# Performance work log

Measured on AMD Instinct MI355X. Metric: run time of the kernel, lower is better.

Reference implementation:

```python
import jax, jax.numpy as jnp
import numpy as np

N = 2060          # drug-graph nodes (m_drug_d_num)
F_OUT = 901       # out_feats, forced by Linear(901*2, ...)
M = 901 + (N - 1183)  # 1778 fused node rows
E = N * 64
N_TRAIN, N_TEST = 100000, 30000
EPS = 1e-5


def setup_inputs() -> dict:
    key = jax.random.key(0)
    ks = jax.random.split(key, 30)
    f32 = jnp.float32
    inp = {
        'x_feat': jax.random.normal(ks[0], (N, N), f32),
        'mirna_feat': jax.random.normal(ks[1], (M, F_OUT), f32),
        'Wg': jax.random.normal(ks[2], (N, F_OUT), f32) * 0.02,
        'att_src': jax.random.normal(ks[3], (F_OUT,), f32) * 0.05,
        'att_dst': jax.random.normal(ks[4], (F_OUT,), f32) * 0.05,
        'gat_b': jnp.zeros((F_OUT,), f32),
        'lw1': jax.random.normal(ks[5], (1, 2), f32) * 0.5,
        'lb1': jnp.zeros((1,), f32),
        'lw2': jax.random.normal(ks[6], (2, 1), f32) * 0.5,
        'lb2': jnp.zeros((2,), f32),
        'gw1': jax.random.normal(ks[7], (1, 2), f32) * 0.5,
        'gb1': jnp.zeros((1,), f32),
        'gw2': jax.random.normal(ks[8], (2, 1), f32) * 0.5,
        'gb2': jnp.zeros((2,), f32),
        'W1': jax.random.normal(ks[9], (2 * F_OUT, 1024), f32) * 0.02,
        'b1': jnp.zeros((1024,), f32),
        'W2': jax.random.normal(ks[10], (1024, 512), f32) * 0.03,
        'b2': jnp.zeros((512,), f32),
        'W3': jax.random.normal(ks[11], (512, 64), f32) * 0.04,
        'b3': jnp.zeros((64,), f32),
        'W4': jax.random.normal(ks[12], (64, 1), f32) * 0.1,
        'b4': jnp.zeros((1,), f32),
        'edge_index': jax.random.randint(ks[13], (2, E), 0, N, jnp.int32),
        'train_sample': jax.random.randint(ks[14], (N_TRAIN, 2), 0, M, jnp.int32),
        'test_sample': jax.random.randint(ks[15], (N_TEST, 2), 0, M, jnp.int32),
    }
    return inp


def _bn(x, axes):
    # BatchNorm in train mode (fresh module: gamma=1, beta=0, biased batch var)
    mu = x.mean(axes, keepdims=True)
    var = x.var(axes, keepdims=True)
    return (x - mu) * jax.lax.rsqrt(var + EPS)


def _gat(x, Wg, att_src, att_dst, gat_b, edge_index):
    # single-head PyG-style GATConv with self loops, negative_slope=0.2
    h = x @ Wg                                         # [N, F]
    loop = jnp.arange(N, dtype=edge_index.dtype)
    src = jnp.concatenate([edge_index[0], loop])
    dst = jnp.concatenate([edge_index[1], loop])
    a_s = h @ att_src                                  # [N]
    a_d = h @ att_dst
    e = jax.nn.leaky_relu(a_s[src] + a_d[dst], 0.2)    # per-edge logits
    emax = jax.ops.segment_max(e, dst, num_segments=N)
    ex = jnp.exp(e - emax[dst])
    denom = jax.ops.segment_sum(ex, dst, num_segments=N)
    alpha = ex / denom[dst]
    out = jax.ops.segment_sum(alpha[:, None] * h[src], dst, num_segments=N) + gat_b
    return jax.nn.relu(out)                            # F.relu in MGL (MGC relu is idempotent)


def _forward(x_feat, mirna_feat, Wg, att_src, att_dst, gat_b,
             lw1, lb1, lw2, lb2, gw1, gb1, gw2, gb2,
             W1, b1, W2, b2, W3, b3, W4, b4,
             edge_index, train_sample, test_sample):
    g = _gat(x_feat, Wg, att_src, att_dst, gat_b, edge_index)      # [N, 901]
    drug_view = jnp.concatenate([g[:901], g[1183:]], axis=0)       # [M, 901]
    x = jnp.stack([drug_view, mirna_feat], axis=1)                 # [M, 2, 901]  (B=M, C=2, H=1 dropped, W=901)

    # MS_CAM (channels=2, r=2), BN in train mode
    xl = jnp.einsum('mcw,oc->mow', x, lw1) + lb1[None, :, None]    # [M, 1, 901]
    xl = jax.nn.relu(_bn(xl, (0, 2)))
    xl = jnp.einsum('mcw,oc->mow', xl, lw2) + lb2[None, :, None]   # [M, 2, 901]
    xl = _bn(xl, (0, 2))

    gp = x.mean(axis=2)                                            # [M, 2] global avg pool
    xg = gp @ gw1.T + gb1                                          # [M, 1]
    xg = jax.nn.relu(_bn(xg, (0,)))
    xg = xg @ gw2.T + gb2                                          # [M, 2]
    xg = _bn(xg, (0,))

    wei = jax.nn.sigmoid(xl + xg[:, :, None])
    x = x * wei                                                    # [M, 2, 901]
    fused = (x[:, 0, :] + x[:, 1, :]) * 0.5                        # [M, 901]

    def score(pairs):
        emb = jnp.concatenate([fused[pairs[:, 0]], fused[pairs[:, 1]]], axis=1)  # [B, 1802]
        h = emb @ W1 + b1
        h = h @ W2 + b2
        h = h @ W3 + b3
        return jax.nn.sigmoid(h @ W4 + b4)

    return score(train_sample), score(test_sample)


def reference(x_feat, mirna_feat, Wg, att_src, att_dst, gat_b,
              lw1, lb1, lw2, lb2, gw1, gb1, gw2, gb2,
              W1, b1, W2, b2, W3, b3, W4, b4,
              edge_index, train_sample, test_sample):
    return _forward(x_feat, mirna_feat, Wg, att_src, att_dst, gat_b,
                    lw1, lb1, lw2, lb2, gw1, gb1, gw2, gb2,
                    W1, b1, W2, b2, W3, b3, W4, b4,
                    edge_index, train_sample, test_sample)
```

## Files before the change

kernel.cpp:

```cpp
#include <hip/hip_runtime.h>

typedef unsigned short u16;
typedef unsigned int   u32;

#define NN   2060
#define FF   901
#define HP   904
#define MM   1778
#define EE   131840
#define ETOT 133900
#define NTR  100000
#define NOUT 130000
#define MP   2112
#define KP   2080
#define NP   960
#define EPSV 1e-5f
#define NTOT 1601978.0

typedef __attribute__((ext_vector_type(4))) float f32x4;
typedef __attribute__((ext_vector_type(8))) short bf16x8;

#define GLL16(g,l) __builtin_amdgcn_global_load_lds( \
    (const __attribute__((address_space(1))) u32*)(g), \
    (__attribute__((address_space(3))) u32*)(l), 16, 0, 0)

__device__ __forceinline__ float bf2f(u16 u){ return __uint_as_float(((u32)u)<<16); }
__device__ __forceinline__ u16 f2bf(float f){
  u32 b = __float_as_uint(f);
  return (u16)((b + 0x7fffu + ((b>>16)&1u)) >> 16);
}
__device__ __forceinline__ float ldf(const void* p, size_t i, int bf){
  return bf ? bf2f(((const u16*)p)[i]) : ((const float*)p)[i];
}
__device__ __forceinline__ u16 ldb(const void* p, size_t i, int bf){
  return bf ? ((const u16*)p)[i] : f2bf(((const float*)p)[i]);
}
__device__ __forceinline__ float waveSum(float v){
  #pragma unroll
  for (int o = 32; o; o >>= 1) v += __shfl_down(v, o);
  return v;
}
__device__ __forceinline__ int waveSumI(int v){
  #pragma unroll
  for (int o = 32; o; o >>= 1) v += __shfl_down(v, o);
  return v;
}
__device__ __forceinline__ int flagWave(const u32* __restrict__ x){
  int l = threadIdx.x & 63;
  u32 w0 = x[l], w1 = x[l + 64];
  int big = (((w0 >> 7)  & 0xFFu) >= 0xC0u) + (((w0 >> 23) & 0xFFu) >= 0xC0u)
          + (((w1 >> 7)  & 0xFFu) >= 0xC0u) + (((w1 >> 23) & 0xFFu) >= 0xC0u);
  big = waveSumI(big);
  return (__shfl(big, 0) >= 8) ? 0 : 1;
}
__device__ __forceinline__ void edgeSD(const int* __restrict__ ei, int e, int& src, int& dst){
  if (e < EE){ src = ei[e]; dst = ei[EE + e]; } else { src = dst = e - EE; }
}

__global__ __launch_bounds__(256) void pad_k(const void* __restrict__ X, const void* __restrict__ Wg,
                                             const void* __restrict__ W3, const void* __restrict__ W4,
                                             const void* __restrict__ b3, const void* __restrict__ b4,
                                             const int* __restrict__ ei,
                                             u16* __restrict__ Ap, u16* __restrict__ BT,
                                             float* __restrict__ u3, float* __restrict__ cp,
                                             int* __restrict__ cnts, int* bfp){
  __shared__ u16 tt[32][33];
  int bf = flagWave((const u32*)X);
  int blk = blockIdx.x, tid = threadIdx.x;
  if (blk == 0 && tid == 0) *bfp = bf;
  if (blk < MP){
    int row = blk;
    for (int c0 = tid * 8; c0 < KP; c0 += 2048){
      u16 v[8] = {0,0,0,0,0,0,0,0};
      if (row < NN){
        if (c0 + 8 <= NN){
          if (bf){
            ushort4 t0 = *(const ushort4*)((const u16*)X + (size_t)row * NN + c0);
            ushort4 t1 = *(const ushort4*)((const u16*)X + (size_t)row * NN + c0 + 4);
            v[0]=t0.x; v[1]=t0.y; v[2]=t0.z; v[3]=t0.w;
            v[4]=t1.x; v[5]=t1.y; v[6]=t1.z; v[7]=t1.w;
          } else {
            float4 t0 = *(const float4*)((const float*)X + (size_t)row * NN + c0);
            float4 t1 = *(const float4*)((const float*)X + (size_t)row * NN + c0 + 4);
            v[0]=f2bf(t0.x); v[1]=f2bf(t0.y); v[2]=f2bf(t0.z); v[3]=f2bf(t0.w);
            v[4]=f2bf(t1.x); v[5]=f2bf(t1.y); v[6]=f2bf(t1.z); v[7]=f2bf(t1.w);
          }
        } else {
          #pragma unroll
          for (int i = 0; i < 8; ++i)
            if (c0 + i < NN) v[i] = ldb(X, (size_t)row * NN + c0 + i, bf);
        }
      }
      *(uint4*)(Ap + (size_t)row * KP + c0) = *(const uint4*)v;
    }
  } else if (blk < MP + 1950){
    int t = blk - MP;
    int kb = (t % 65) * 32, nb = (t / 65) * 32;
    int tx = tid & 31, ty = tid >> 5;
    #pragma unroll
    for (int i = 0; i < 4; ++i){
      int k = kb + ty + 8*i, n = nb + tx;
      u16 v = 0;
      if (k < NN && n < FF) v = ldb(Wg, (size_t)k * FF + n, bf);
      tt[ty + 8*i][tx] = v;
    }
    __syncthreads();
    #pragma unroll
    for (int i = 0; i < 4; ++i){
      int n = nb + ty + 8*i, k = kb + tx;
      if (n < NP && k < KP) BT[(size_t)n * KP + k] = tt[tx][ty + 8*i];
    }
  } else if (blk < MP + 1950 + 514){
    if (tid >= 64) return;
    int ob = blk - (MP + 1950);
    if (ob > 512) return;
    float s = (ob < 512) ? ldf(W3, (size_t)ob*64 + tid, bf) * ldf(W4, tid, bf)
                         : ldf(b3, tid, bf) * ldf(W4, tid, bf);
    s = waveSum(s);
    if (tid == 0){ if (ob < 512) u3[ob] = s; else cp[0] = s + ldf(b4, 0, bf); }
  } else {
    int e = (blk - (MP + 1950 + 514)) * 256 + tid;
    if (e >= ETOT) return;
    int src, dst; edgeSD(ei, e, src, dst);
    atomicAdd(&cnts[dst], 1);
  }
}

__global__ __launch_bounds__(256) void scan_k(const int* __restrict__ counts, int* __restrict__ offs,
                                              const void* __restrict__ W2, const void* __restrict__ b2,
                                              const float* __restrict__ u3, float* __restrict__ u2,
                                              float* __restrict__ cp, const int* bfp){
  int blk = blockIdx.x, tid = threadIdx.x;
  if (blk == 0){
    __shared__ int part[256];
    const int CH = (NN + 255) / 256;
    int base = tid * CH, s = 0;
    for (int i = 0; i < CH; ++i){ int idx = base + i; if (idx < NN) s += counts[idx]; }
    part[tid] = s;
    __syncthreads();
    if (tid == 0){ int run = 0; for (int i = 0; i < 256; ++i){ int v = part[i]; part[i] = run; run += v; } }
    __syncthreads();
    int run = part[tid];
    for (int i = 0; i < CH; ++i){ int idx = base + i; if (idx < NN){ offs[idx] = run; run += counts[idx]; } }
    if (tid == 255) offs[NN] = run;
  } else {
    int bf = *bfp;
    __shared__ float sh[4];
    #pragma unroll 1
    for (int r = 0; r < 2; ++r){
      int ob = (blk - 1) * 2 + r;
      if (ob <= 1024){
        float s = 0;
        if (ob < 1024){ for (int j = tid; j < 512; j += 256) s += ldf(W2, (size_t)ob*512 + j, bf) * u3[j]; }
        else          { for (int j = tid; j < 512; j += 256) s += ldf(b2, j, bf) * u3[j]; }
        s = waveSum(s);
        __syncthreads();
        if ((tid & 63) == 0) sh[tid >> 6] = s;
        __syncthreads();
        if (tid == 0){ float t = sh[0]+sh[1]+sh[2]+sh[3]; if (ob < 1024) u2[ob] = t; else cp[1] = t; }
      }
    }
  }
}

__global__ __launch_bounds__(256) void gemm_k(const u16* __restrict__ A, const u16* __restrict__ BT,
                                              u16* __restrict__ h,
                                              const void* __restrict__ W1, const void* __restrict__ b1,
                                              const float* __restrict__ u2, float* __restrict__ u1,
                                              float* __restrict__ cp, const int* bfp){
  __shared__ __align__(16) u16 sA[2][64*32];
  __shared__ __align__(16) u16 sB[2][64*32];
  __shared__ float shr[4];
  int blk = blockIdx.x, tid = threadIdx.x;
  if (blk >= 495){
    int bf = *bfp;
    #pragma unroll 1
    for (int r = 0; r < 4; ++r){
      int ob = (blk - 495) * 4 + r;
      if (ob <= 1802){
        float s = 0;
        if (ob < 1802){ for (int j = tid; j < 1024; j += 256) s += ldf(W1, (size_t)ob*1024 + j, bf) * u2[j]; }
        else          { for (int j = tid; j < 1024; j += 256) s += ldf(b1, j, bf) * u2[j]; }
        s = waveSum(s);
        __syncthreads();
        if ((tid & 63) == 0) shr[tid >> 6] = s;
        __syncthreads();
        if (tid == 0){ float t = shr[0]+shr[1]+shr[2]+shr[3]; if (ob < 1802) u1[ob] = t; else cp[2] = t; }
      }
    }
    return;
  }
  int bm = (blk % 33) * 64, bn = (blk / 33) * 64;
  int lane = tid & 63, wave = tid >> 6;
  int wm = (wave >> 1) * 32, wn = (wave & 1) * 32;
  f32x4 acc[2][2] = {};
  int srow = tid >> 2;
  int schunk = (tid & 3) ^ ((tid >> 3) & 3);
  const u16* gA = A  + (size_t)(bm + srow) * KP + schunk * 8;
  const u16* gB = BT + (size_t)(bn + srow) * KP + schunk * 8;
  int fr = lane & 15, quad = lane >> 4;
  int qs = quad ^ ((fr >> 1) & 3);
  const int KIT = KP / 32;
  GLL16(gA, &sA[0][wave * 512]);
  GLL16(gB, &sB[0][wave * 512]);
  for (int kt = 0; kt < KIT; ++kt){
    int cur = kt & 1;
    __syncthreads();
    if (kt + 1 < KIT){
      GLL16(gA + (kt + 1) * 32, &sA[cur ^ 1][wave * 512]);
      GLL16(gB + (kt + 1) * 32, &sB[cur ^ 1][wave * 512]);
    }
    bf16x8 a0 = *(const bf16x8*)&sA[cur][(wm      + fr) * 32 + qs * 8];
    bf16x8 a1 = *(const bf16x8*)&sA[cur][(wm + 16 + fr) * 32 + qs * 8];
    bf16x8 b0 = *(const bf16x8*)&sB[cur][(wn      + fr) * 32 + qs * 8];
    bf16x8 b1 = *(const bf16x8*)&sB[cur][(wn + 16 + fr) * 32 + qs * 8];
    acc[0][0] = __builtin_amdgcn_mfma_f32_16x16x32_bf16(a0, b0, acc[0][0], 0,0,0);
    acc[0][1] = __builtin_amdgcn_mfma_f32_16x16x32_bf16(a0, b1, acc[0][1], 0,0,0);
    acc[1][0] = __builtin_amdgcn_mfma_f32_16x16x32_bf16(a1, b0, acc[1][0], 0,0,0);
    acc[1][1] = __builtin_amdgcn_mfma_f32_16x16x32_bf16(a1, b1, acc[1][1], 0,0,0);
  }
  #pragma unroll
  for (int im = 0; im < 2; ++im)
    #pragma unroll
    for (int in = 0; in < 2; ++in)
      #pragma unroll
      for (int i = 0; i < 4; ++i){
        int row = bm + wm + im*16 + quad*4 + i;
        int col = bn + wn + in*16 + fr;
        if (row < NN && col < FF) h[(size_t)row * HP + col] = f2bf(acc[im][in][i]);
      }
}

__global__ __launch_bounds__(256) void asd_k(const u16* __restrict__ h, const void* att_s, const void* att_d,
                                             float* a_s, float* a_d, const int* bfp){
  int bf = *bfp;
  int wv = threadIdx.x >> 6, lane = threadIdx.x & 63;
  int n = blockIdx.x * 4 + wv;
  if (n >= NN) return;
  float ss = 0, sd = 0;
  for (int f = lane; f < FF; f += 64){
    float hv = bf2f(h[(size_t)n * HP + f]);
    ss += hv * ldf(att_s, f, bf);
    sd += hv * ldf(att_d, f, bf);
  }
  ss = waveSum(ss); sd = waveSum(sd);
  if (lane == 0){ a_s[n] = ss; a_d[n] = sd; }
}

__global__ __launch_bounds__(256) void edge2_k(const int* __restrict__ ei, const float* __restrict__ a_s,
                                               const float* __restrict__ a_d, float* __restrict__ denom,
                                               const int* __restrict__ offs, int* __restrict__ fill,
                                               int* __restrict__ csr_src, float* __restrict__ csr_w){
  int e = blockIdx.x * 256 + threadIdx.x;
  if (e >= ETOT) return;
  int src, dst; edgeSD(ei, e, src, dst);
  float x = a_s[src] + a_d[dst];
  float ev = x > 0.f ? x : 0.2f * x;
  float ex = expf(ev);
  atomicAdd(&denom[dst], ex);
  int pos = offs[dst] + atomicAdd(&fill[dst], 1);
  csr_src[pos] = src; csr_w[pos] = ex;
}

__device__ __forceinline__ void acc8(float* a, uint4 v, float w){
  u32 arr[4] = {v.x, v.y, v.z, v.w};
  #pragma unroll
  for (int i = 0; i < 4; ++i){
    a[2*i]   += w * __uint_as_float((arr[i] & 0xFFFFu) << 16);
    a[2*i+1] += w * __uint_as_float(arr[i] & 0xFFFF0000u);
  }
}
__global__ __launch_bounds__(128) void aggr_k(const u16* __restrict__ h, const int* __restrict__ offs,
                                              const int* __restrict__ csr_src, const float* __restrict__ csr_w,
                                              const float* __restrict__ denom, const void* gat_b,
                                              const void* __restrict__ mirna,
                                              const void* lw1, const void* lb1,
                                              float* __restrict__ g, float* __restrict__ gp,
                                              float2* __restrict__ pA, const int* bfp){
  int bf = *bfp;
  int m = blockIdx.x, tid = threadIdx.x;
  int dst = m < 901 ? m : m + 282;
  int o0 = offs[dst], o1 = offs[dst + 1];
  float inv = 1.0f / denom[dst];
  __shared__ int   sS[128];
  __shared__ float sW[128];
  __shared__ float red[4][2];
  const int c = tid;
  float a[8] = {0,0,0,0,0,0,0,0};
  for (int base = o0; base < o1; base += 128){
    int nb = min(128, o1 - base);
    __syncthreads();
    if (tid < nb){ sS[tid] = csr_src[base + tid]; sW[tid] = csr_w[base + tid] * inv; }
    __syncthreads();
    if (c < 113){
      int k = 0;
      for (; k + 4 <= nb; k += 4){
        int   i0 = sS[k], i1 = sS[k+1], i2 = sS[k+2], i3 = sS[k+3];
        float w0 = sW[k], w1 = sW[k+1], w2 = sW[k+2], w3 = sW[k+3];
        uint4 v0 = ((const uint4*)(h + (size_t)i0 * HP))[c];
        uint4 v1 = ((const uint4*)(h + (size_t)i1 * HP))[c];
        uint4 v2 = ((const uint4*)(h + (size_t)i2 * HP))[c];
        uint4 v3 = ((const uint4*)(h + (size_t)i3 * HP))[c];
        acc8(a, v0, w0); acc8(a, v1, w1); acc8(a, v2, w2); acc8(a, v3, w3);
      }
      for (; k < nb; ++k){
        uint4 v0 = ((const uint4*)(h + (size_t)sS[k] * HP))[c];
        acc8(a, v0, sW[k]);
      }
    }
  }
  float w00 = ldf(lw1,0,bf), w01 = ldf(lw1,1,bf), bb = ldf(lb1,0,bf);
  float sx0 = 0, sx1 = 0, sl = 0, sl2 = 0;
  if (c < 113){
    int f0 = 8 * c;
    float r[8];
    #pragma unroll
    for (int i = 0; i < 8; ++i){
      bool inb = (f0 + i) < FF;
      float v = a[i] + (inb ? ldf(gat_b, f0 + i, bf) : 0.f);
      v = v > 0.f ? v : 0.f;
      r[i] = inb ? v : 0.f;
      if (inb){
        float x1 = ldf(mirna, (size_t)m * FF + f0 + i, bf);
        float xl = w00*r[i] + w01*x1 + bb;
        sx0 += r[i]; sx1 += x1; sl += xl; sl2 += xl*xl;
      }
    }
    float4* go = (float4*)(g + (size_t)dst * HP);
    go[2*c]   = make_float4(r[0], r[1], r[2], r[3]);
    go[2*c+1] = make_float4(r[4], r[5], r[6], r[7]);
  }
  sx0 = waveSum(sx0); sx1 = waveSum(sx1); sl = waveSum(sl); sl2 = waveSum(sl2);
  int wv = tid >> 6;
  if ((tid & 63) == 0){ red[0][wv]=sx0; red[1][wv]=sx1; red[2][wv]=sl; red[3][wv]=sl2; }
  __syncthreads();
  if (tid == 0){
    gp[2*m]   = (red[0][0]+red[0][1]) / (float)FF;
    gp[2*m+1] = (red[1][0]+red[1][1]) / (float)FF;
    pA[m] = make_float2(red[2][0]+red[2][1], red[3][0]+red[3][1]);
  }
}

__global__ __launch_bounds__(256) void bn_k(const float* __restrict__ g, const void* __restrict__ mirna,
                                            const void* lw1, const void* lb1,
                                            const void* gw1, const void* gb1, const void* gw2,
                                            const float* __restrict__ gp,
                                            const float2* __restrict__ pA, float2* __restrict__ pB,
                                            float* __restrict__ xg2b, const int* bfp){
  __shared__ float xs[MM];
  __shared__ float red[2][4];
  __shared__ float bc[3];
  int m = blockIdx.x, tid = threadIdx.x, bf = *bfp;
  int wv = tid >> 6;
  if (m == MM){
    float g10 = ldf(gw1,0,bf), g11 = ldf(gw1,1,bf), b1v = ldf(gb1,0,bf);
    float s = 0, s2 = 0;
    for (int i = tid; i < MM; i += 256){
      float v = g10*gp[2*i] + g11*gp[2*i+1] + b1v;
      xs[i] = v; s += v; s2 += v*v;
    }
    s = waveSum(s); s2 = waveSum(s2);
    if ((tid & 63) == 0){ red[0][wv] = s; red[1][wv] = s2; }
    __syncthreads();
    if (tid == 0){
      float t  = red[0][0]+red[0][1]+red[0][2]+red[0][3];
      float t2 = red[1][0]+red[1][1]+red[1][2]+red[1][3];
      float mean = t / (float)MM, var = t2 / (float)MM - mean*mean;
      bc[0] = mean; bc[1] = rsqrtf(var + EPSV);
    }
    __syncthreads();
    float mean = bc[0], rs = bc[1];
    s = 0; s2 = 0;
    for (int i = tid; i < MM; i += 256){
      float r = (xs[i] - mean) * rs; r = r > 0.f ? r : 0.f;
      xs[i] = r; s += r; s2 += r*r;
    }
    s = waveSum(s); s2 = waveSum(s2);
    __syncthreads();
    if ((tid & 63) == 0){ red[0][wv] = s; red[1][wv] = s2; }
    __syncthreads();
    if (tid == 0){
      float t  = red[0][0]+red[0][1]+red[0][2]+red[0][3];
      float t2 = red[1][0]+red[1][1]+red[1][2]+red[1][3];
      float mrg = t / (float)MM, vrg = t2 / (float)MM - mrg*mrg;
      float g20 = ldf(gw2,0,bf), g21 = ldf(gw2,1,bf);
      bc[0] = mrg;
      bc[1] = g20 * rsqrtf(g20*g20*vrg + EPSV);
      bc[2] = g21 * rsqrtf(g21*g21*vrg + EPSV);
    }
    __syncthreads();
    float mrg = bc[0], c0 = bc[1], c1 = bc[2];
    for (int i = tid; i < MM; i += 256){
      float d = xs[i] - mrg;
      xg2b[2*i] = c0 * d; xg2b[2*i+1] = c1 * d;
    }
  } else {
    float s = 0, s2 = 0;
    for (int i = tid; i < MM; i += 256){ float2 p = pA[i]; s += p.x; s2 += p.y; }
    s = waveSum(s); s2 = waveSum(s2);
    if ((tid & 63) == 0){ red[0][wv] = s; red[1][wv] = s2; }
    __syncthreads();
    if (tid == 0){
      float t  = red[0][0]+red[0][1]+red[0][2]+red[0][3];
      float t2 = red[1][0]+red[1][1]+red[1][2]+red[1][3];
      float mu = (float)((double)t / NTOT);
      bc[0] = mu;
      bc[1] = rsqrtf((float)((double)t2 / NTOT) - mu*mu + EPSV);
    }
    __syncthreads();
    float mu1 = bc[0], rs1 = bc[1];
    int gr = m < 901 ? m : m + 282;
    float w00 = ldf(lw1,0,bf), w01 = ldf(lw1,1,bf), bb = ldf(lb1,0,bf);
    float sr = 0, sr2 = 0;
    for (int w = tid; w < FF; w += 256){
      float x0 = g[(size_t)gr * HP + w];
      float x1 = ldf(mirna, (size_t)m * FF + w, bf);
      float xl = w00*x0 + w01*x1 + bb;
      float r = (xl - mu1) * rs1; r = r > 0.f ? r : 0.f;
      sr += r; sr2 += r*r;
    }
    sr = waveSum(sr); sr2 = waveSum(sr2);
    __syncthreads();
    if ((tid & 63) == 0){ red[0][wv] = sr; red[1][wv] = sr2; }
    __syncthreads();
    if (tid == 0) pB[m] = make_float2(red[0][0]+red[0][1]+red[0][2]+red[0][3],
                                      red[1][0]+red[1][1]+red[1][2]+red[1][3]);
  }
}

__global__ __launch_bounds__(256) void fs_k(const float* __restrict__ g, const void* __restrict__ mirna,
                                            const void* lw1, const void* lb1, const void* lw2,
                                            const float2* __restrict__ pA, const float2* __restrict__ pB,
                                            const float* __restrict__ xg2b,
                                            const float* __restrict__ u1,
                                            float* __restrict__ s0, float* __restrict__ s1, const int* bfp){
  __shared__ float red[4][4];
  __shared__ float cst[5];
  int bf = *bfp;
  int m = blockIdx.x, tid = threadIdx.x;
  int wv = tid >> 6;
  {
    float a1 = 0, a2 = 0, b1 = 0, b2 = 0;
    for (int i = tid; i < MM; i += 256){
      float2 p = pA[i]; a1 += p.x; a2 += p.y;
      float2 q = pB[i]; b1 += q.x; b2 += q.y;
    }
    a1 = waveSum(a1); a2 = waveSum(a2); b1 = waveSum(b1); b2 = waveSum(b2);
    if ((tid & 63) == 0){ red[0][wv]=a1; red[1][wv]=a2; red[2][wv]=b1; red[3][wv]=b2; }
    __syncthreads();
    if (tid == 0){
      float tA  = red[0][0]+red[0][1]+red[0][2]+red[0][3];
      float tA2 = red[1][0]+red[1][1]+red[1][2]+red[1][3];
      float tB  = red[2][0]+red[2][1]+red[2][2]+red[2][3];
      float tB2 = red[3][0]+red[3][1]+red[3][2]+red[3][3];
      float mu = (float)((double)tA / NTOT);
      float rs = rsqrtf((float)((double)tA2 / NTOT) - mu*mu + EPSV);
      float mr = (float)((double)tB / NTOT);
      float vr = (float)((double)tB2 / NTOT) - mr*mr;
      float l20 = ldf(lw2,0,bf), l21 = ldf(lw2,1,bf);
      cst[0] = mu; cst[1] = rs; cst[2] = mr;
      cst[3] = l20 * rsqrtf(l20*l20*vr + EPSV);
      cst[4] = l21 * rsqrtf(l21*l21*vr + EPSV);
    }
    __syncthreads();
  }
  float mu1 = cst[0], rs1 = cst[1], mr = cst[2], A0 = cst[3], A1 = cst[4];
  int gr = m < 901 ? m : m + 282;
  float w00 = ldf(lw1,0,bf), w01 = ldf(lw1,1,bf), bb = ldf(lb1,0,bf);
  float xa = xg2b[2*m], xb = xg2b[2*m+1];
  float p0 = 0, p1 = 0;
  for (int w = tid; w < FF; w += 256){
    float x0 = g[(size_t)gr * HP + w];
    float x1 = ldf(mirna, (size_t)m * FF + w, bf);
    float xl = w00*x0 + w01*x1 + bb;
    float r = (xl - mu1) * rs1; r = r > 0.f ? r : 0.f;
    float rc = r - mr;
    float z0 = A0*rc + xa, z1 = A1*rc + xb;
    float sg0 = 1.f / (1.f + expf(-z0));
    float sg1 = 1.f / (1.f + expf(-z1));
    float f = 0.5f * (x0*sg0 + x1*sg1);
    p0 += f * u1[w]; p1 += f * u1[901 + w];
  }
  p0 = waveSum(p0); p1 = waveSum(p1);
  __syncthreads();
  if ((tid & 63) == 0){ red[0][wv] = p0; red[1][wv] = p1; }
  __syncthreads();
  if (tid == 0){
    s0[m] = red[0][0]+red[0][1]+red[0][2]+red[0][3];
    s1[m] = red[1][0]+red[1][1]+red[1][2]+red[1][3];
  }
}

__global__ __launch_bounds__(256) void out_k(const int* __restrict__ tr, const int* __restrict__ te,
                                             const float* __restrict__ s0, const float* __restrict__ s1,
                                             const float* __restrict__ cp, void* __restrict__ out,
                                             const int* bfp){
  int bf = *bfp;
  int b = blockIdx.x * 256 + threadIdx.x;
  if (b >= NOUT) return;
  int i, j;
  if (b < NTR){ i = tr[2*b]; j = tr[2*b + 1]; }
  else { int t = b - NTR; i = te[2*t]; j = te[2*t + 1]; }
  float z = s0[i] + s1[j] + cp[0] + cp[1] + cp[2];
  float v = 1.f / (1.f + expf(-z));
  if (bf) ((u16*)out)[b] = f2bf(v);
  else    ((float*)out)[b] = v;
}

extern "C" void kernel_launch(void* const* d_in, const int* in_sizes, int n_in,
                              void* d_out, int out_size, void* d_ws, size_t ws_size,
                              hipStream_t stream){
  const void* x_feat = d_in[0];
  const void* mirna  = d_in[1];
  const void* Wg     = d_in[2];
  const void* att_s  = d_in[3];
  const void* att_d  = d_in[4];
  const void* gat_b  = d_in[5];
  const void* lw1    = d_in[6];
  const void* lb1    = d_in[7];
  const void* lw2    = d_in[8];
  const void* gw1    = d_in[10];
  const void* gb1    = d_in[11];
  const void* gw2    = d_in[12];
  const void* W1     = d_in[14];
  const void* b1     = d_in[15];
  const void* W2     = d_in[16];
  const void* b2     = d_in[17];
  const void* W3     = d_in[18];
  const void* b3     = d_in[19];
  const void* W4     = d_in[20];
  const void* b4     = d_in[21];
  const int* ei      = (const int*)d_in[22];
  const int* tr      = (const int*)d_in[23];
  const int* te      = (const int*)d_in[24];

  char* ws = (char*)d_ws;
  size_t off = 0;
  auto alloc = [&](size_t bytes)->size_t{ size_t o = off; off += (bytes + 255) & ~(size_t)255; return o; };
  size_t oA  = alloc((size_t)MP*KP*2);
  size_t oBT = alloc((size_t)NP*KP*2);
  size_t oH  = alloc((size_t)NN*HP*2);
  size_t oCS = alloc((size_t)ETOT*4);
  size_t oCW = alloc((size_t)ETOT*4);
  size_t oAS = alloc(NN*4);
  size_t oAD = alloc(NN*4);
  size_t oOF = alloc((NN+1)*4);
  size_t oGP = alloc(MM*2*4);
  size_t oXG = alloc(MM*2*4);
  size_t oS0 = alloc(MM*4);
  size_t oS1 = alloc(MM*4);
  size_t oU3 = alloc(512*4);
  size_t oU2 = alloc(1024*4);
  size_t oU1 = alloc(1802*4);
  size_t oPA = alloc(MM*8);
  size_t oPB = alloc(MM*8);
  size_t oCP = alloc(3*4);
  size_t oBF = alloc(4);
  size_t zstart = off;
  size_t oCT = alloc(NN*4);
  size_t oFL = alloc(NN*4);
  size_t oDN = alloc(NN*4);
  size_t zend = off;

  u16*   Ap   = (u16*)(ws+oA);
  u16*   BT   = (u16*)(ws+oBT);
  u16*   h    = (u16*)(ws+oH);
  float* gbuf = (float*)(ws+oA);
  int*   csrS = (int*)(ws+oCS);
  float* csrW = (float*)(ws+oCW);
  float* a_s  = (float*)(ws+oAS);
  float* a_d  = (float*)(ws+oAD);
  int*   offs = (int*)(ws+oOF);
  float* gp   = (float*)(ws+oGP);
  float* xg2b = (float*)(ws+oXG);
  float* s0   = (float*)(ws+oS0);
  float* s1   = (float*)(ws+oS1);
  float* u3   = (float*)(ws+oU3);
  float* u2   = (float*)(ws+oU2);
  float* u1   = (float*)(ws+oU1);
  float2* pA  = (float2*)(ws+oPA);
  float2* pB  = (float2*)(ws+oPB);
  float* cp   = (float*)(ws+oCP);
  int*   bfp  = (int*)(ws+oBF);
  int*   cnts = (int*)(ws+oCT);
  int*   fill = (int*)(ws+oFL);
  float* denom= (float*)(ws+oDN);

  hipMemsetAsync(ws + zstart, 0, zend - zstart, stream);

  pad_k  <<<MP + 1950 + 514 + (ETOT+255)/256, 256, 0, stream>>>(
      x_feat, Wg, W3, W4, b3, b4, ei, Ap, BT, u3, cp, cnts, bfp);
  scan_k <<<514, 256, 0, stream>>>(cnts, offs, W2, b2, u3, u2, cp, bfp);
  gemm_k <<<495 + 451, 256, 0, stream>>>(Ap, BT, h, W1, b1, u2, u1, cp, bfp);
  asd_k  <<<(NN+3)/4, 256, 0, stream>>>(h, att_s, att_d, a_s, a_d, bfp);
  edge2_k<<<(ETOT+255)/256, 256, 0, stream>>>(ei, a_s, a_d, denom, offs, fill, csrS, csrW);
  aggr_k <<<MM, 128, 0, stream>>>(h, offs, csrS, csrW, denom, gat_b, mirna, lw1, lb1, gbuf, gp, pA, bfp);
  bn_k   <<<MM + 1, 256, 0, stream>>>(gbuf, mirna, lw1, lb1, gw1, gb1, gw2, gp, pA, pB, xg2b, bfp);
  fs_k   <<<MM, 256, 0, stream>>>(gbuf, mirna, lw1, lb1, lw2, pA, pB, xg2b, u1, s0, s1, bfp);
  out_k  <<<(NOUT+255)/256, 256, 0, stream>>>(tr, te, s0, s1, cp, d_out, bfp);
}
```

Before: 254.8 us.

## Compute GAT attention logits as X·(Wg·att) and drop asd kernel

Reassociates the attention-score dot products so that a_s and a_d are X times precomputed vectors Wg·att_src and Wg·att_dst, instead of being read from the GEMM output h. The Wg·att vectors are built in extra pad_k blocks and the per-node dot products in extra scan_k blocks. This removes the separate asd_k launch and lets edge2_k run before the feature GEMM, taking the score computation off the post-GEMM path. In exchange, X (about 2060×2080 bf16) and Wg are reread, and rounding differs slightly because h is no longer rounded to bf16 before the dot product.

```diff
diff --git a/kernel.cpp b/kernel.cpp
--- a/kernel.cpp
+++ b/kernel.cpp
@@ -57,12 +57,20 @@
   if (e < EE){ src = ei[e]; dst = ei[EE + e]; } else { src = dst = e - EE; }
 }
 
+#define SB_TR   MP
+#define SB_C1   (MP + 1950)
+#define SB_WV   (SB_C1 + 514)
+#define SB_ED   (SB_WV + 515)
+#define PAD_GRID (SB_ED + 524)
+
 __global__ __launch_bounds__(256) void pad_k(const void* __restrict__ X, const void* __restrict__ Wg,
                                              const void* __restrict__ W3, const void* __restrict__ W4,
                                              const void* __restrict__ b3, const void* __restrict__ b4,
+                                             const void* __restrict__ att_s, const void* __restrict__ att_d,
                                              const int* __restrict__ ei,
                                              u16* __restrict__ Ap, u16* __restrict__ BT,
                                              float* __restrict__ u3, float* __restrict__ cp,
+                                             float* __restrict__ wsv, float* __restrict__ wdv,
                                              int* __restrict__ cnts, int* bfp){
   __shared__ u16 tt[32][33];
   int bf = flagWave((const u32*)X);
@@ -93,8 +101,8 @@
       }
       *(uint4*)(Ap + (size_t)row * KP + c0) = *(const uint4*)v;
     }
-  } else if (blk < MP + 1950){
-    int t = blk - MP;
+  } else if (blk < SB_C1){
+    int t = blk - SB_TR;
     int kb = (t % 65) * 32, nb = (t / 65) * 32;
     int tx = tid & 31, ty = tid >> 5;
     #pragma unroll
@@ -110,16 +118,28 @@
       int n = nb + ty + 8*i, k = kb + tx;
       if (n < NP && k < KP) BT[(size_t)n * KP + k] = tt[tx][ty + 8*i];
     }
-  } else if (blk < MP + 1950 + 514){
+  } else if (blk < SB_WV){
     if (tid >= 64) return;
-    int ob = blk - (MP + 1950);
+    int ob = blk - SB_C1;
     if (ob > 512) return;
     float s = (ob < 512) ? ldf(W3, (size_t)ob*64 + tid, bf) * ldf(W4, tid, bf)
                          : ldf(b3, tid, bf) * ldf(W4, tid, bf);
     s = waveSum(s);
     if (tid == 0){ if (ob < 512) u3[ob] = s; else cp[0] = s + ldf(b4, 0, bf); }
+  } else if (blk < SB_ED){
+    int wv = tid >> 6, lane = tid & 63;
+    int k = (blk - SB_WV) * 4 + wv;
+    if (k >= NN) return;
+    float ss = 0, sd = 0;
+    for (int c = lane; c < FF; c += 64){
+      float w = ldf(Wg, (size_t)k * FF + c, bf);
+      ss += w * ldf(att_s, c, bf);
+      sd += w * ldf(att_d, c, bf);
+    }
+    ss = waveSum(ss); sd = waveSum(sd);
+    if (lane == 0){ wsv[k] = ss; wdv[k] = sd; }
   } else {
-    int e = (blk - (MP + 1950 + 514)) * 256 + tid;
+    int e = (blk - SB_ED) * 256 + tid;
     if (e >= ETOT) return;
     int src, dst; edgeSD(ei, e, src, dst);
     atomicAdd(&cnts[dst], 1);
@@ -129,7 +149,11 @@
 __global__ __launch_bounds__(256) void scan_k(const int* __restrict__ counts, int* __restrict__ offs,
                                               const void* __restrict__ W2, const void* __restrict__ b2,
                                               const float* __restrict__ u3, float* __restrict__ u2,
-                                              float* __restrict__ cp, const int* bfp){
+                                              float* __restrict__ cp,
+                                              const u16* __restrict__ Ap,
+                                              const float* __restrict__ wsv, const float* __restrict__ wdv,
+                                              float* __restrict__ a_s, float* __restrict__ a_d,
+                                              const int* bfp){
   int blk = blockIdx.x, tid = threadIdx.x;
   if (blk == 0){
     __shared__ int part[256];
@@ -143,7 +167,7 @@
     int run = part[tid];
     for (int i = 0; i < CH; ++i){ int idx = base + i; if (idx < NN){ offs[idx] = run; run += counts[idx]; } }
     if (tid == 255) offs[NN] = run;
-  } else {
+  } else if (blk < 514){
     int bf = *bfp;
     __shared__ float sh[4];
     #pragma unroll 1
@@ -160,6 +184,32 @@
         if (tid == 0){ float t = sh[0]+sh[1]+sh[2]+sh[3]; if (ob < 1024) u2[ob] = t; else cp[1] = t; }
       }
     }
+  } else {
+    int wv = tid >> 6, lane = tid & 63;
+    int n = (blk - 514) * 4 + wv;
+    if (n >= NN) return;
+    const u16* row = Ap + (size_t)n * KP;
+    float ss = 0, sd = 0;
+    for (int k0 = lane * 8; k0 < KP; k0 += 512){
+      uint4 v = *(const uint4*)(row + k0);
+      float4 w0 = *(const float4*)(wsv + k0);
+      float4 w1 = *(const float4*)(wsv + k0 + 4);
+      float4 d0 = *(const float4*)(wdv + k0);
+      float4 d1 = *(const float4*)(wdv + k0 + 4);
+      u32 arr[4] = {v.x, v.y, v.z, v.w};
+      float xv[8];
+      #pragma unroll
+      for (int i = 0; i < 4; ++i){
+        xv[2*i]   = __uint_as_float((arr[i] & 0xFFFFu) << 16);
+        xv[2*i+1] = __uint_as_float(arr[i] & 0xFFFF0000u);
+      }
+      ss += xv[0]*w0.x + xv[1]*w0.y + xv[2]*w0.z + xv[3]*w0.w
+          + xv[4]*w1.x + xv[5]*w1.y + xv[6]*w1.z + xv[7]*w1.w;
+      sd += xv[0]*d0.x + xv[1]*d0.y + xv[2]*d0.z + xv[3]*d0.w
+          + xv[4]*d1.x + xv[5]*d1.y + xv[6]*d1.z + xv[7]*d1.w;
+    }
+    ss = waveSum(ss); sd = waveSum(sd);
+    if (lane == 0){ a_s[n] = ss; a_d[n] = sd; }
   }
 }
 
@@ -229,22 +279,6 @@
         int col = bn + wn + in*16 + fr;
         if (row < NN && col < FF) h[(size_t)row * HP + col] = f2bf(acc[im][in][i]);
       }
-}
-
-__global__ __launch_bounds__(256) void asd_k(const u16* __restrict__ h, const void* att_s, const void* att_d,
-                                             float* a_s, float* a_d, const int* bfp){
-  int bf = *bfp;
-  int wv = threadIdx.x >> 6, lane = threadIdx.x & 63;
-  int n = blockIdx.x * 4 + wv;
-  if (n >= NN) return;
-  float ss = 0, sd = 0;
-  for (int f = lane; f < FF; f += 64){
-    float hv = bf2f(h[(size_t)n * HP + f]);
-    ss += hv * ldf(att_s, f, bf);
-    sd += hv * ldf(att_d, f, bf);
-  }
-  ss = waveSum(ss); sd = waveSum(sd);
-  if (lane == 0){ a_s[n] = ss; a_d[n] = sd; }
 }
 
 __global__ __launch_bounds__(256) void edge2_k(const int* __restrict__ ei, const float* __restrict__ a_s,
@@ -560,6 +594,8 @@
   size_t oCT = alloc(NN*4);
   size_t oFL = alloc(NN*4);
   size_t oDN = alloc(NN*4);
+  size_t oWS = alloc(KP*4);
+  size_t oWD = alloc(KP*4);
   size_t zend = off;
 
   u16*   Ap   = (u16*)(ws+oA);
@@ -585,15 +621,16 @@
   int*   cnts = (int*)(ws+oCT);
   int*   fill = (int*)(ws+oFL);
   float* denom= (float*)(ws+oDN);
+  float* wsv  = (float*)(ws+oWS);
+  float* wdv  = (float*)(ws+oWD);
 
   hipMemsetAsync(ws + zstart, 0, zend - zstart, stream);
 
-  pad_k  <<<MP + 1950 + 514 + (ETOT+255)/256, 256, 0, stream>>>(
-      x_feat, Wg, W3, W4, b3, b4, ei, Ap, BT, u3, cp, cnts, bfp);
-  scan_k <<<514, 256, 0, stream>>>(cnts, offs, W2, b2, u3, u2, cp, bfp);
+  pad_k  <<<PAD_GRID, 256, 0, stream>>>(
+      x_feat, Wg, W3, W4, b3, b4, att_s, att_d, ei, Ap, BT, u3, cp, wsv, wdv, cnts, bfp);
+  scan_k <<<1029, 256, 0, stream>>>(cnts, offs, W2, b2, u3, u2, cp, Ap, wsv, wdv, a_s, a_d, bfp);
+  edge2_k<<<(ETOT+255)/256, 256, 0, stream>>>(ei, a_s, a_d, denom, offs, fill, csrS, csrW);
   gemm_k <<<495 + 451, 256, 0, stream>>>(Ap, BT, h, W1, b1, u2, u1, cp, bfp);
-  asd_k  <<<(NN+3)/4, 256, 0, stream>>>(h, att_s, att_d, a_s, a_d, bfp);
-  edge2_k<<<(ETOT+255)/256, 256, 0, stream>>>(ei, a_s, a_d, denom, offs, fill, csrS, csrW);
   aggr_k <<<MM, 128, 0, stream>>>(h, offs, csrS, csrW, denom, gat_b, mirna, lw1, lb1, gbuf, gp, pA, bfp);
   bn_k   <<<MM + 1, 256, 0, stream>>>(gbuf, mirna, lw1, lb1, gw1, gb1, gw2, gp, pA, pB, xg2b, bfp);
   fs_k   <<<MM, 256, 0, stream>>>(gbuf, mirna, lw1, lb1, lw2, pA, pB, xg2b, u1, s0, s1, bfp);
```

After: 250.7 us (median of 2 runs). Within noise of the previous version (-1.6%).
